# Performance work log

Hardware: AMD Instinct MI355X
Metric: run time of the kernel (lower is better)

## Reference

```python
import jax, jax.numpy as jnp
import numpy as np

LABEL_SIZE = 50
NUM_LABELS = LABEL_SIZE + 2  # + start, end
START = NUM_LABELS - 2
END = NUM_LABELS - 1
NEG = -100.0


def setup_inputs() -> dict:
    key = jax.random.key(0)
    k1, k2, k3, k4, k5 = jax.random.split(key, 5)
    B, S, D = 128, 512, 1024
    inputs = jax.random.normal(k1, (B, S, D), dtype=jnp.float32)
    lens = jax.random.randint(k2, (B,), 1, S + 1)
    labels = jax.random.randint(k3, (B, S), 0, LABEL_SIZE)
    # Linear: uniform(-bias, bias) with bias = sqrt(6/(out+in))
    bound = np.sqrt(6.0 / (LABEL_SIZE + D))
    W = jax.random.uniform(k4, (LABEL_SIZE, D), minval=-bound, maxval=bound, dtype=jnp.float32)
    b = jnp.zeros((LABEL_SIZE,), dtype=jnp.float32)
    transition = jax.random.normal(k5, (NUM_LABELS, NUM_LABELS), dtype=jnp.float32)
    # transition[to, from]; disallow from=END (column) and to=START (row)
    transition = transition.at[:, END].set(NEG)
    transition = transition.at[START, :].set(NEG)
    return {"inputs": inputs, "W": W, "b": b, "transition": transition,
            "lens": lens, "labels": labels}


def _crf_loss(inputs, W, b, transition, lens, labels):
    B, S, D = inputs.shape
    # emission scores (B, S, label_size) -> padded to (B, S, NUM_LABELS)
    logits = jnp.einsum('bsd,ld->bsl', inputs, W) + b
    logits = jnp.concatenate(
        [logits, jnp.full((B, S, 2), NEG, dtype=logits.dtype)], axis=-1)
    mask = jnp.arange(S)[None, :] < lens[:, None]  # (B, S)

    # ---- norm score: forward algorithm over time (scan) ----
    alpha0 = jnp.full((B, NUM_LABELS), NEG, dtype=logits.dtype).at[:, START].set(0.0)

    def step(alpha, xs):
        logit_t, m_t = xs  # (B, L), (B,)
        # mat[b, j, i] = alpha[b, i] + transition[j, i] + logit_t[b, j]
        mat = alpha[:, None, :] + transition[None, :, :] + logit_t[:, :, None]
        alpha_nxt = jax.nn.logsumexp(mat, axis=2)
        alpha = jnp.where(m_t[:, None], alpha_nxt, alpha)
        return alpha, None

    xs = (jnp.swapaxes(logits, 0, 1), jnp.swapaxes(mask, 0, 1))
    alpha, _ = jax.lax.scan(step, alpha0, xs)
    norm_score = jax.nn.logsumexp(alpha + transition[END][None, :], axis=1)  # (B,)

    # ---- gold score ----
    # unary: emission at gold labels
    unary = jnp.take_along_axis(logits, labels[:, :, None], axis=2)[..., 0]
    unary_score = jnp.sum(unary * mask, axis=1)
    # binary: start -> y1 -> ... -> y_len -> end
    labels_ext = jnp.concatenate(
        [jnp.full((B, 1), START, dtype=labels.dtype), labels,
         jnp.full((B, 1), END, dtype=labels.dtype)], axis=1)  # (B, S+2)
    valid = jnp.arange(S + 2)[None, :] < (lens + 1)[:, None]
    labels_ext = jnp.where(valid, labels_ext, END)
    pair = transition[labels_ext[:, 1:], labels_ext[:, :-1]]  # (B, S+1)
    pair_mask = jnp.arange(S + 1)[None, :] < (lens + 1)[:, None]
    binary_score = jnp.sum(pair * pair_mask, axis=1)

    gold_score = unary_score + binary_score
    return -jnp.sum(gold_score - norm_score)


def reference(inputs, W, b, transition, lens, labels):
    return _crf_loss(inputs, W, b, transition, lens, labels)
```

## Files before the change

kernel.cpp:

```cpp
#include <hip/hip_runtime.h>
#include <stdint.h>

#define LBL 50
#define NL 52
#define L2E 1.4426950408889634f
#define BB 128
#define SS 512
#define DD 1024

typedef __attribute__((ext_vector_type(8))) short short8;
typedef __attribute__((ext_vector_type(4))) float float4v;
typedef __attribute__((ext_vector_type(2))) float float2v;

union S8U { unsigned int u[4]; short8 s; };

static __device__ __forceinline__ unsigned int f2bf(float f) {
    union { float f; unsigned int u; } v; v.f = f;
    unsigned int r = v.u + 0x7fffu + ((v.u >> 16) & 1u);
    return r >> 16;
}

__global__ __launch_bounds__(256) void wconv(
    const float* __restrict__ W, unsigned short* __restrict__ Wbf)
{
    int i = blockIdx.x * 256 + threadIdx.x;
    int r = i >> 10, c = i & 1023;
    float v = (r < LBL) ? W[r * DD + c] : 0.f;
    Wbf[i] = (unsigned short)f2bf(v);
}

__global__ __launch_bounds__(256) void gemm_pe(
    const float* __restrict__ A,
    const unsigned short* __restrict__ Wbf,
    const float* __restrict__ bias,
    float* __restrict__ PEp)
{
    const int tid  = threadIdx.x;
    const int lane = tid & 63;
    const int wv   = tid >> 6;
    const int mrow = lane & 15;
    const int quad = lane >> 4;
    const int row  = blockIdx.x * 64 + wv * 16 + mrow;

    const uint4* arow = (const uint4*)(A + (size_t)row * DD);

    float4v acc[4];
#pragma unroll
    for (int i = 0; i < 4; ++i) acc[i] = (float4v){0.f, 0.f, 0.f, 0.f};

#pragma unroll 4
    for (int kc = 0; kc < DD; kc += 32) {
        uint4 u0 = arow[(kc >> 2) + quad * 2];
        uint4 u1 = arow[(kc >> 2) + quad * 2 + 1];
        S8U a;
        a.u[0] = __builtin_amdgcn_perm(u0.y, u0.x, 0x07060302u);
        a.u[1] = __builtin_amdgcn_perm(u0.w, u0.z, 0x07060302u);
        a.u[2] = __builtin_amdgcn_perm(u1.y, u1.x, 0x07060302u);
        a.u[3] = __builtin_amdgcn_perm(u1.w, u1.z, 0x07060302u);
#pragma unroll
        for (int nt = 0; nt < 4; ++nt) {
            short8 bf = *(const short8*)(Wbf + (size_t)(nt * 16 + mrow) * DD + kc + quad * 8);
            acc[nt] = __builtin_amdgcn_mfma_f32_16x16x32_bf16(a.s, bf, acc[nt], 0, 0, 0);
        }
    }
    const int r0 = blockIdx.x * 64 + wv * 16 + quad * 4;
#pragma unroll
    for (int nt = 0; nt < 4; ++nt) {
        int col = nt * 16 + mrow;
        float bv = (col < LBL) ? bias[col] : 0.f;
#pragma unroll
        for (int rr = 0; rr < 4; ++rr) {
            float val = (col < LBL) ? __builtin_amdgcn_exp2f((acc[nt][rr] + bv) * L2E) : 0.f;
            PEp[(size_t)(r0 + rr) * 64 + col] = val;
        }
    }
}

__global__ __launch_bounds__(128) void crf_fwd(
    const float* __restrict__ PE,
    const float* __restrict__ T,
    const int*   __restrict__ lens,
    const int*   __restrict__ labels,
    float* __restrict__ out)
{
    const int g    = blockIdx.x;
    const int tid  = threadIdx.x;
    const int lane = tid & 63;
    const int wv   = tid >> 6;
    const int b    = lane & 15;
    const int q    = lane >> 4;

    __shared__ float gold_sh[16];
    float norm_e = 0.f;

    if (wv == 0) {
        const int bb   = g * 16 + b;
        const int lenl = lens[bb];

        short8 afr[4][2];
#pragma unroll
        for (int it = 0; it < 4; ++it) {
            int i = (b >> 2) * 8 + (b & 3) + 4 * (it & 1) + 32 * (it >> 1);
#pragma unroll
            for (int jt = 0; jt < 2; ++jt) {
                S8U pk;
#pragma unroll
                for (int h = 0; h < 4; ++h) {
                    int k0 = jt * 32 + q * 8 + 2 * h;
                    float v0 = (i < NL && k0     < NL) ? __builtin_amdgcn_exp2f(T[i * NL + k0]     * L2E) : 0.f;
                    float v1 = (i < NL && k0 + 1 < NL) ? __builtin_amdgcn_exp2f(T[i * NL + k0 + 1] * L2E) : 0.f;
                    pk.u[h] = f2bf(v0) | (f2bf(v1) << 16);
                }
                afr[it][jt] = pk.s;
            }
        }

        const int addrB = b * 4;

        const float4* lb = (const float4*)(PE + (size_t)bb * SS * 64 + q * 8);

#define LOADP4(dst, trow) do {                                           \
        const float4* _p = lb + (size_t)(trow) * 16;                     \
        float4 _a0 = _p[0], _a1 = _p[1], _a2 = _p[8], _a3 = _p[9];       \
        dst[0]=_a0.x;  dst[1]=_a0.y;  dst[2]=_a0.z;  dst[3]=_a0.w;       \
        dst[4]=_a1.x;  dst[5]=_a1.y;  dst[6]=_a1.z;  dst[7]=_a1.w;       \
        dst[8]=_a2.x;  dst[9]=_a2.y;  dst[10]=_a2.z; dst[11]=_a2.w;      \
        dst[12]=_a3.x; dst[13]=_a3.y; dst[14]=_a3.z; dst[15]=_a3.w;      \
    } while (0)

        float E[16];
        {
            float p0[16];
            LOADP4(p0, 0);
#pragma unroll
            for (int k = 0; k < 16; ++k) {
                int it = k >> 2, r = k & 3;
                int i = q * 8 + r + 4 * (it & 1) + 32 * (it >> 1);
                float ets = (i < NL) ? __builtin_amdgcn_exp2f(T[i * NL + LBL] * L2E) : 0.f;
                E[k] = p0[k] * ets;
            }
        }

        float r0[16], r1[16], r2[16], r3[16];
        LOADP4(r0, 1); LOADP4(r1, 2); LOADP4(r2, 3); LOADP4(r3, 4);

        float ncap = 1.0f;
        int lcap = 0, lsum = 0, ebp = 127;

#define STEP(PC, t) do {                                                          \
                    \
        S8U bfr[2];                                                               \
        _Pragma("unroll")                                                         \
        for (int jt = 0; jt < 2; ++jt) {                                          \
            _Pragma("unroll")                                                     \
            for (int u = 0; u < 4; ++u) {                                         \
                bfr[jt].u[u] = __builtin_amdgcn_perm(                             \
                    __float_as_uint(E[jt * 8 + 2 * u + 1]),                       \
                    __float_as_uint(E[jt * 8 + 2 * u]), 0x07060302u);             \
            }                                                                     \
        }                                                                         \
        const float4v zz = (float4v){0.f, 0.f, 0.f, 0.f};                         \
        float4v acc[4];                                                           \
        _Pragma("unroll")                                                         \
        for (int it = 0; it < 4; ++it) {                                          \
            float4v a0 = __builtin_amdgcn_mfma_f32_16x16x32_bf16(afr[it][0], bfr[0].s, zz, 0, 0, 0); \
            acc[it]    = __builtin_amdgcn_mfma_f32_16x16x32_bf16(afr[it][1], bfr[1].s, a0, 0, 0, 0); \
        }                                                                         \
        bool cap = ((t) == lenl);                                                 \
        ncap = cap ? acc[2][3] : ncap;      \
        lcap = cap ? lsum : lcap;                                                 \
        float s = __uint_as_float((unsigned int)(254 - ebp) << 23);               \
        lsum += 127 - ebp;                                                        \
        int myeb = (int)((__float_as_uint(acc[0][0]) >> 23) & 0xffu);             \
        ebp = __builtin_amdgcn_ds_bpermute(addrB, myeb);                          \
        float2v s2 = (float2v){s, s};                                             \
        _Pragma("unroll")                                                         \
        for (int h = 0; h < 8; ++h) {                                             \
            float2v d2 = (float2v){acc[h>>1][(h&1)*2], acc[h>>1][(h&1)*2+1]};     \
            float2v p2 = (float2v){PC[2*h], PC[2*h+1]};                           \
            float2v e2 = d2 * p2 * s2;                                            \
            E[2*h] = e2.x; E[2*h+1] = e2.y;                                       \
        }                                                                         \
        int _tn = (t) + 4; _tn = (_tn < SS) ? _tn : (SS - 1);                     \
        LOADP4(PC, _tn);                                                          \
    } while (0)

        for (int t0 = 1; t0 <= SS; t0 += 4) {
            STEP(r0, t0);
            STEP(r1, t0 + 1);
            STEP(r2, t0 + 2);
            STEP(r3, t0 + 3);
        }
#undef STEP
#undef LOADP4

        norm_e = (__builtin_amdgcn_logf(ncap) - (float)lcap) * (1.0f / L2E);
    } else {
        const int lb2 = lane >> 2;
        const int ph  = lane & 3;
        const int bb  = g * 16 + lb2;
        const int len = lens[bb];
        const size_t base = (size_t)bb * SS;
        float un2 = 0.f, bi = 0.f;
        for (int t = ph; t < len; t += 4) {
            int lab = labels[base + t];
            un2 += __builtin_amdgcn_logf(PE[(base + t) * 64 + lab]);
            int prev = (t == 0) ? LBL : labels[base + t - 1];
            bi += T[lab * NL + prev];
        }
        float gsum = un2 * (1.0f / L2E) + bi;
        gsum += __shfl_xor(gsum, 1, 64);
        gsum += __shfl_xor(gsum, 2, 64);
        if (ph == 0) {
            gsum += T[(NL - 1) * NL + labels[base + len - 1]];
            gold_sh[lb2] = gsum;
        }
    }

    __syncthreads();
    if (wv == 0 && q == 2) {
        float v = norm_e - gold_sh[b];
        v += __shfl_xor(v, 1, 64);
        v += __shfl_xor(v, 2, 64);
        v += __shfl_xor(v, 4, 64);
        v += __shfl_xor(v, 8, 64);
        if (b == 0) atomicAdd(out, v);
    }
}

extern "C" void kernel_launch(void* const* d_in, const int* in_sizes, int n_in,
                              void* d_out, int out_size, void* d_ws, size_t ws_size,
                              hipStream_t stream) {
    const float* A      = (const float*)d_in[0];
    const float* W      = (const float*)d_in[1];
    const float* bias   = (const float*)d_in[2];
    const float* T      = (const float*)d_in[3];
    const int*   lens   = (const int*)d_in[4];
    const int*   labels = (const int*)d_in[5];
    float* out = (float*)d_out;

    float* PEp = (float*)d_ws;
    unsigned short* Wbf = (unsigned short*)((char*)d_ws + (size_t)65536 * 64 * 4);

    hipMemsetAsync(d_out, 0, sizeof(float), stream);
    wconv<<<dim3(256), dim3(256), 0, stream>>>(W, Wbf);
    gemm_pe<<<dim3((BB * SS) / 64), dim3(256), 0, stream>>>(A, Wbf, bias, PEp);
    crf_fwd<<<dim3(8), dim3(128), 0, stream>>>(PEp, T, lens, labels, out);
}
```

Measured before the change: 492.4 us.

## Parallelize CRF forward scan via segmented matrix products and combine pass

Replaces the serial 512-step forward recursion, which ran on only 8 blocks, with a parallel-in-time scheme. Each of 2048 single-wave blocks computes the 64x64 product of the scaled transition-emission matrices over a 32-step segment of one sequence, storing it in bf16 plus an exponent correction. A second kernel then folds the 16 segment matrices per sequence as vector-matrix products starting from the END row, and computes the gold score in parallel. This does far more arithmetic (full matrix-matrix products instead of matrix-vector) and rounds intermediate products to bf16, in exchange for filling the GPU instead of leaving a long serial chain on a few CUs.

```diff
diff --git a/kernel.cpp b/kernel.cpp
--- a/kernel.cpp
+++ b/kernel.cpp
@@ -10,7 +10,6 @@
 
 typedef __attribute__((ext_vector_type(8))) short short8;
 typedef __attribute__((ext_vector_type(4))) float float4v;
-typedef __attribute__((ext_vector_type(2))) float float2v;
 
 union S8U { unsigned int u[4]; short8 s; };
 
@@ -76,156 +75,242 @@
     }
 }
 
-__global__ __launch_bounds__(128) void crf_fwd(
+__global__ __launch_bounds__(64) void crf_seg(
+    const float* __restrict__ PE,
+    const float* __restrict__ T,
+    const int*   __restrict__ lens,
+    unsigned short* __restrict__ segm,
+    int* __restrict__ segc)
+{
+    const int sk   = blockIdx.x;
+    const int s    = sk >> 4;
+    const int k    = sk & 15;
+    const int lane = threadIdx.x & 63;
+    const int b    = lane & 15;
+    const int q    = lane >> 4;
+    const int L    = lens[s];
+    const int t0   = 1 + k * 32;
+    int tend = t0 + 31; if (L - 1 < tend) tend = L - 1;
+
+    short8 afr[4][2];
+#pragma unroll
+    for (int it = 0; it < 4; ++it) {
+        int i = (b >> 2) * 8 + (b & 3) + 4 * (it & 1) + 32 * (it >> 1);
+#pragma unroll
+        for (int jt = 0; jt < 2; ++jt) {
+            S8U pk;
+#pragma unroll
+            for (int h = 0; h < 4; ++h) {
+                int k0 = jt * 32 + q * 8 + 2 * h;
+                float v0 = (i < NL && k0     < NL) ? __builtin_amdgcn_exp2f(T[i * NL + k0]     * L2E) : 0.f;
+                float v1 = (i < NL && k0 + 1 < NL) ? __builtin_amdgcn_exp2f(T[i * NL + k0 + 1] * L2E) : 0.f;
+                pk.u[h] = f2bf(v0) | (f2bf(v1) << 16);
+            }
+            afr[it][jt] = pk.s;
+        }
+    }
+
+    S8U bfr[4][2];
+#pragma unroll
+    for (int nt = 0; nt < 4; ++nt)
+#pragma unroll
+        for (int kc = 0; kc < 2; ++kc)
+#pragma unroll
+            for (int u = 0; u < 4; ++u) {
+                int kk = kc * 32 + q * 8 + 2 * u;
+                int n  = nt * 16 + b;
+                unsigned int v = 0;
+                if (kk == n)     v |= 0x3F80u;
+                if (kk + 1 == n) v |= (0x3F80u << 16);
+                bfr[nt][kc].u[u] = v;
+            }
+
+    int csum = 0;
+    if (t0 <= tend) {
+        const float* prow = PE + (size_t)(s * SS + t0) * 64 + q * 8;
+        float4 f0 = *(const float4*)(prow);
+        float4 f1 = *(const float4*)(prow + 4);
+        float4 f2 = *(const float4*)(prow + 32);
+        float4 f3 = *(const float4*)(prow + 36);
+        for (int t = t0; t <= tend; ++t) {
+            const float* pn = prow + 64;
+            float4 g0 = *(const float4*)(pn);
+            float4 g1 = *(const float4*)(pn + 4);
+            float4 g2 = *(const float4*)(pn + 32);
+            float4 g3 = *(const float4*)(pn + 36);
+
+            const float4v zz = (float4v){0.f, 0.f, 0.f, 0.f};
+            float4v acc[4][4];
+#pragma unroll
+            for (int it = 0; it < 4; ++it)
+#pragma unroll
+                for (int nt = 0; nt < 4; ++nt)
+                    acc[it][nt] = __builtin_amdgcn_mfma_f32_16x16x32_bf16(afr[it][0], bfr[nt][0].s, zz, 0, 0, 0);
+#pragma unroll
+            for (int it = 0; it < 4; ++it)
+#pragma unroll
+                for (int nt = 0; nt < 4; ++nt)
+                    acc[it][nt] = __builtin_amdgcn_mfma_f32_16x16x32_bf16(afr[it][1], bfr[nt][1].s, acc[it][nt], 0, 0, 0);
+
+            int myeb = (int)((__float_as_uint(acc[0][0][0]) >> 23) & 0xffu);
+            int eb   = __builtin_amdgcn_readfirstlane(myeb);
+            float ss = __uint_as_float((unsigned int)(254 - eb) << 23);
+            csum += 127 - eb;
+
+            float pvs[16];
+            pvs[0]  = f0.x * ss; pvs[1]  = f0.y * ss; pvs[2]  = f0.z * ss; pvs[3]  = f0.w * ss;
+            pvs[4]  = f1.x * ss; pvs[5]  = f1.y * ss; pvs[6]  = f1.z * ss; pvs[7]  = f1.w * ss;
+            pvs[8]  = f2.x * ss; pvs[9]  = f2.y * ss; pvs[10] = f2.z * ss; pvs[11] = f2.w * ss;
+            pvs[12] = f3.x * ss; pvs[13] = f3.y * ss; pvs[14] = f3.z * ss; pvs[15] = f3.w * ss;
+
+#pragma unroll
+            for (int nt = 0; nt < 4; ++nt) {
+                float ev[16];
+#pragma unroll
+                for (int kp = 0; kp < 16; ++kp)
+                    ev[kp] = acc[kp >> 2][nt][kp & 3] * pvs[kp];
+#pragma unroll
+                for (int kc = 0; kc < 2; ++kc)
+#pragma unroll
+                    for (int u = 0; u < 4; ++u)
+                        bfr[nt][kc].u[u] = __builtin_amdgcn_perm(
+                            __float_as_uint(ev[kc * 8 + 2 * u + 1]),
+                            __float_as_uint(ev[kc * 8 + 2 * u]), 0x07060302u);
+            }
+
+            f0 = g0; f1 = g1; f2 = g2; f3 = g3;
+            prow = pn;
+        }
+    }
+
+    unsigned short* ob = segm + (size_t)sk * 4096;
+#pragma unroll
+    for (int nt = 0; nt < 4; ++nt)
+#pragma unroll
+        for (int kc = 0; kc < 2; ++kc) {
+            uint4 st; st.x = bfr[nt][kc].u[0]; st.y = bfr[nt][kc].u[1];
+            st.z = bfr[nt][kc].u[2]; st.w = bfr[nt][kc].u[3];
+            *(uint4*)(ob + (nt * 16 + b) * 64 + kc * 32 + q * 8) = st;
+        }
+    if (lane == 0) segc[sk] = csum;
+}
+
+__global__ __launch_bounds__(128) void crf_comb(
     const float* __restrict__ PE,
     const float* __restrict__ T,
     const int*   __restrict__ lens,
     const int*   __restrict__ labels,
+    const unsigned short* __restrict__ segm,
+    const int*   __restrict__ segc,
     float* __restrict__ out)
 {
-    const int g    = blockIdx.x;
+    const int s    = blockIdx.x;
     const int tid  = threadIdx.x;
     const int lane = tid & 63;
     const int wv   = tid >> 6;
-    const int b    = lane & 15;
-    const int q    = lane >> 4;
-
-    __shared__ float gold_sh[16];
-    float norm_e = 0.f;
-
-    if (wv == 0) {
-        const int bb   = g * 16 + b;
-        const int lenl = lens[bb];
-
-        short8 afr[4][2];
-#pragma unroll
-        for (int it = 0; it < 4; ++it) {
-            int i = (b >> 2) * 8 + (b & 3) + 4 * (it & 1) + 32 * (it >> 1);
-#pragma unroll
-            for (int jt = 0; jt < 2; ++jt) {
-                S8U pk;
-#pragma unroll
-                for (int h = 0; h < 4; ++h) {
-                    int k0 = jt * 32 + q * 8 + 2 * h;
-                    float v0 = (i < NL && k0     < NL) ? __builtin_amdgcn_exp2f(T[i * NL + k0]     * L2E) : 0.f;
-                    float v1 = (i < NL && k0 + 1 < NL) ? __builtin_amdgcn_exp2f(T[i * NL + k0 + 1] * L2E) : 0.f;
-                    pk.u[h] = f2bf(v0) | (f2bf(v1) << 16);
+
+    __shared__ float gold_sh;
+    float norm_ln = 0.f;
+
+    if (wv == 1) {
+        const int len = lens[s];
+        const size_t base = (size_t)s * SS;
+        float un2 = 0.f, bi = 0.f;
+        for (int t = lane; t < len; t += 64) {
+            int lab  = labels[base + t];
+            int prev = (t == 0) ? LBL : labels[base + t - 1];
+            un2 += __builtin_amdgcn_logf(PE[(base + t) * 64 + lab]);
+            bi  += T[lab * NL + prev];
+        }
+        float g = un2 * (1.0f / L2E) + bi;
+        g += __shfl_xor(g, 1, 64);
+        g += __shfl_xor(g, 2, 64);
+        g += __shfl_xor(g, 4, 64);
+        g += __shfl_xor(g, 8, 64);
+        g += __shfl_xor(g, 16, 64);
+        g += __shfl_xor(g, 32, 64);
+        if (lane == 0) {
+            g += T[(NL - 1) * NL + labels[base + len - 1]];
+            gold_sh = g;
+        }
+    } else {
+        const int b = lane & 15, q = lane >> 4;
+        const float4v zz = (float4v){0.f, 0.f, 0.f, 0.f};
+
+        S8U aw[2];
+#pragma unroll
+        for (int kc = 0; kc < 2; ++kc)
+#pragma unroll
+            for (int u = 0; u < 4; ++u) {
+                int j0 = kc * 32 + q * 8 + 2 * u;
+                float v0 = (j0     < NL) ? __builtin_amdgcn_exp2f(T[(NL - 1) * NL + j0]     * L2E) : 0.f;
+                float v1 = (j0 + 1 < NL) ? __builtin_amdgcn_exp2f(T[(NL - 1) * NL + j0 + 1] * L2E) : 0.f;
+                aw[kc].u[u] = f2bf(v0) | (f2bf(v1) << 16);
+            }
+
+        int F = 0;
+        float sv0 = 0.f, sv1 = 0.f, sv2 = 0.f, sv3 = 0.f;
+
+        for (int kk = 15; kk >= 0; --kk) {
+            const unsigned short* mb = segm + (size_t)(s * 16 + kk) * 4096;
+            S8U bfr[4][2];
+#pragma unroll
+            for (int nt = 0; nt < 4; ++nt)
+#pragma unroll
+                for (int kc = 0; kc < 2; ++kc) {
+                    uint4 ld = *(const uint4*)(mb + (nt * 16 + b) * 64 + kc * 32 + q * 8);
+                    bfr[nt][kc].u[0] = ld.x; bfr[nt][kc].u[1] = ld.y;
+                    bfr[nt][kc].u[2] = ld.z; bfr[nt][kc].u[3] = ld.w;
                 }
-                afr[it][jt] = pk.s;
-            }
-        }
-
-        const int addrB = b * 4;
-
-        const float4* lb = (const float4*)(PE + (size_t)bb * SS * 64 + q * 8);
-
-#define LOADP4(dst, trow) do {                                           \
-        const float4* _p = lb + (size_t)(trow) * 16;                     \
-        float4 _a0 = _p[0], _a1 = _p[1], _a2 = _p[8], _a3 = _p[9];       \
-        dst[0]=_a0.x;  dst[1]=_a0.y;  dst[2]=_a0.z;  dst[3]=_a0.w;       \
-        dst[4]=_a1.x;  dst[5]=_a1.y;  dst[6]=_a1.z;  dst[7]=_a1.w;       \
-        dst[8]=_a2.x;  dst[9]=_a2.y;  dst[10]=_a2.z; dst[11]=_a2.w;      \
-        dst[12]=_a3.x; dst[13]=_a3.y; dst[14]=_a3.z; dst[15]=_a3.w;      \
-    } while (0)
-
-        float E[16];
-        {
-            float p0[16];
-            LOADP4(p0, 0);
-#pragma unroll
-            for (int k = 0; k < 16; ++k) {
-                int it = k >> 2, r = k & 3;
-                int i = q * 8 + r + 4 * (it & 1) + 32 * (it >> 1);
-                float ets = (i < NL) ? __builtin_amdgcn_exp2f(T[i * NL + LBL] * L2E) : 0.f;
-                E[k] = p0[k] * ets;
-            }
-        }
-
-        float r0[16], r1[16], r2[16], r3[16];
-        LOADP4(r0, 1); LOADP4(r1, 2); LOADP4(r2, 3); LOADP4(r3, 4);
-
-        float ncap = 1.0f;
-        int lcap = 0, lsum = 0, ebp = 127;
-
-#define STEP(PC, t) do {                                                          \
-                    \
-        S8U bfr[2];                                                               \
-        _Pragma("unroll")                                                         \
-        for (int jt = 0; jt < 2; ++jt) {                                          \
-            _Pragma("unroll")                                                     \
-            for (int u = 0; u < 4; ++u) {                                         \
-                bfr[jt].u[u] = __builtin_amdgcn_perm(                             \
-                    __float_as_uint(E[jt * 8 + 2 * u + 1]),                       \
-                    __float_as_uint(E[jt * 8 + 2 * u]), 0x07060302u);             \
-            }                                                                     \
-        }                                                                         \
-        const float4v zz = (float4v){0.f, 0.f, 0.f, 0.f};                         \
-        float4v acc[4];                                                           \
-        _Pragma("unroll")                                                         \
-        for (int it = 0; it < 4; ++it) {                                          \
-            float4v a0 = __builtin_amdgcn_mfma_f32_16x16x32_bf16(afr[it][0], bfr[0].s, zz, 0, 0, 0); \
-            acc[it]    = __builtin_amdgcn_mfma_f32_16x16x32_bf16(afr[it][1], bfr[1].s, a0, 0, 0, 0); \
-        }                                                                         \
-        bool cap = ((t) == lenl);                                                 \
-        ncap = cap ? acc[2][3] : ncap;      \
-        lcap = cap ? lsum : lcap;                                                 \
-        float s = __uint_as_float((unsigned int)(254 - ebp) << 23);               \
-        lsum += 127 - ebp;                                                        \
-        int myeb = (int)((__float_as_uint(acc[0][0]) >> 23) & 0xffu);             \
-        ebp = __builtin_amdgcn_ds_bpermute(addrB, myeb);                          \
-        float2v s2 = (float2v){s, s};                                             \
-        _Pragma("unroll")                                                         \
-        for (int h = 0; h < 8; ++h) {                                             \
-            float2v d2 = (float2v){acc[h>>1][(h&1)*2], acc[h>>1][(h&1)*2+1]};     \
-            float2v p2 = (float2v){PC[2*h], PC[2*h+1]};                           \
-            float2v e2 = d2 * p2 * s2;                                            \
-            E[2*h] = e2.x; E[2*h+1] = e2.y;                                       \
-        }                                                                         \
-        int _tn = (t) + 4; _tn = (_tn < SS) ? _tn : (SS - 1);                     \
-        LOADP4(PC, _tn);                                                          \
-    } while (0)
-
-        for (int t0 = 1; t0 <= SS; t0 += 4) {
-            STEP(r0, t0);
-            STEP(r1, t0 + 1);
-            STEP(r2, t0 + 2);
-            STEP(r3, t0 + 3);
-        }
-#undef STEP
-#undef LOADP4
-
-        norm_e = (__builtin_amdgcn_logf(ncap) - (float)lcap) * (1.0f / L2E);
-    } else {
-        const int lb2 = lane >> 2;
-        const int ph  = lane & 3;
-        const int bb  = g * 16 + lb2;
-        const int len = lens[bb];
-        const size_t base = (size_t)bb * SS;
-        float un2 = 0.f, bi = 0.f;
-        for (int t = ph; t < len; t += 4) {
-            int lab = labels[base + t];
-            un2 += __builtin_amdgcn_logf(PE[(base + t) * 64 + lab]);
-            int prev = (t == 0) ? LBL : labels[base + t - 1];
-            bi += T[lab * NL + prev];
-        }
-        float gsum = un2 * (1.0f / L2E) + bi;
-        gsum += __shfl_xor(gsum, 1, 64);
-        gsum += __shfl_xor(gsum, 2, 64);
-        if (ph == 0) {
-            gsum += T[(NL - 1) * NL + labels[base + len - 1]];
-            gold_sh[lb2] = gsum;
-        }
+            float4v acc[4];
+#pragma unroll
+            for (int nt = 0; nt < 4; ++nt)
+                acc[nt] = __builtin_amdgcn_mfma_f32_16x16x32_bf16(aw[0].s, bfr[nt][0].s, zz, 0, 0, 0);
+#pragma unroll
+            for (int nt = 0; nt < 4; ++nt)
+                acc[nt] = __builtin_amdgcn_mfma_f32_16x16x32_bf16(aw[1].s, bfr[nt][1].s, acc[nt], 0, 0, 0);
+
+            int myeb = (int)((__float_as_uint(acc[0][0]) >> 23) & 0xffu);
+            int eb   = __builtin_amdgcn_readfirstlane(myeb);
+            float ssc = __uint_as_float((unsigned int)(254 - eb) << 23);
+            F += segc[s * 16 + kk] + (127 - eb);
+
+            sv0 = acc[0][0] * ssc; sv1 = acc[1][0] * ssc;
+            sv2 = acc[2][0] * ssc; sv3 = acc[3][0] * ssc;
+
+            if (kk == 0) break;
+
+            float svq = (q & 2) ? ((q & 1) ? sv3 : sv2) : ((q & 1) ? sv1 : sv0);
+            int svqi = __float_as_int(svq);
+#pragma unroll
+            for (int kc = 0; kc < 2; ++kc)
+#pragma unroll
+                for (int u = 0; u < 4; ++u) {
+                    int j0 = kc * 32 + q * 8 + 2 * u;
+                    int w0i = __builtin_amdgcn_ds_bpermute(j0 * 4,       svqi);
+                    int w1i = __builtin_amdgcn_ds_bpermute((j0 + 1) * 4, svqi);
+                    aw[kc].u[u] = __builtin_amdgcn_perm((unsigned)w1i, (unsigned)w0i, 0x07060302u);
+                }
+        }
+
+        float dp = 0.f;
+        const float* pe0 = PE + (size_t)s * SS * 64;
+        float svs[4] = {sv0, sv1, sv2, sv3};
+#pragma unroll
+        for (int nt = 0; nt < 4; ++nt) {
+            int n = nt * 16 + b;
+            float e1 = (n < NL) ? pe0[n] * __builtin_amdgcn_exp2f(T[n * NL + LBL] * L2E) : 0.f;
+            dp += svs[nt] * e1;
+        }
+        dp += __shfl_xor(dp, 1, 64);
+        dp += __shfl_xor(dp, 2, 64);
+        dp += __shfl_xor(dp, 4, 64);
+        dp += __shfl_xor(dp, 8, 64);
+        norm_ln = (__builtin_amdgcn_logf(dp) - (float)F) * (1.0f / L2E);
     }
 
     __syncthreads();
-    if (wv == 0 && q == 2) {
-        float v = norm_e - gold_sh[b];
-        v += __shfl_xor(v, 1, 64);
-        v += __shfl_xor(v, 2, 64);
-        v += __shfl_xor(v, 4, 64);
-        v += __shfl_xor(v, 8, 64);
-        if (b == 0) atomicAdd(out, v);
-    }
+    if (tid == 0) atomicAdd(out, norm_ln - gold_sh);
 }
 
 extern "C" void kernel_launch(void* const* d_in, const int* in_sizes, int n_in,
@@ -240,10 +325,13 @@
     float* out = (float*)d_out;
 
     float* PEp = (float*)d_ws;
-    unsigned short* Wbf = (unsigned short*)((char*)d_ws + (size_t)65536 * 64 * 4);
+    unsigned short* Wbf  = (unsigned short*)((char*)d_ws + (size_t)65536 * 64 * 4);
+    unsigned short* segm = (unsigned short*)((char*)d_ws + ((size_t)32 << 20));
+    int*            segc = (int*)((char*)d_ws + ((size_t)56 << 20));
 
     hipMemsetAsync(d_out, 0, sizeof(float), stream);
     wconv<<<dim3(256), dim3(256), 0, stream>>>(W, Wbf);
     gemm_pe<<<dim3((BB * SS) / 64), dim3(256), 0, stream>>>(A, Wbf, bias, PEp);
-    crf_fwd<<<dim3(8), dim3(128), 0, stream>>>(PEp, T, lens, labels, out);
-}
+    crf_seg<<<dim3(2048), dim3(64), 0, stream>>>(PEp, T, lens, segm, segc);
+    crf_comb<<<dim3(128), dim3(128), 0, stream>>>(PEp, T, lens, labels, segm, segc, out);
+}
```

Result: faster. 442.3 us (-10.2%).
